# Optimization experiments

Hardware: AMD Instinct MI355X
Metric: run time of the kernel (lower is better)

Reference implementation:

```python
import jax, jax.numpy as jnp
import numpy as np

NUM_HEADS = 8
WEIGHTS_DIM = 512
INPUT_DIM = 512
D_HEAD = WEIGHTS_DIM // NUM_HEADS


def setup_inputs() -> dict:
    key = jax.random.key(0)
    ks = jax.random.split(key, 9)
    B, S, D = 4, 2048, INPUT_DIM
    s_in = 1.0 / np.sqrt(D)
    s_w = 1.0 / np.sqrt(WEIGHTS_DIM)
    return {
        "x": jax.random.normal(ks[0], (B, S, D), dtype=jnp.float32),
        "Wq": jax.random.normal(ks[1], (D, WEIGHTS_DIM), dtype=jnp.float32) * s_in,
        "bq": jnp.zeros((WEIGHTS_DIM,), dtype=jnp.float32),
        "Wk": jax.random.normal(ks[2], (D, WEIGHTS_DIM), dtype=jnp.float32) * s_in,
        "bk": jnp.zeros((WEIGHTS_DIM,), dtype=jnp.float32),
        "Wv": jax.random.normal(ks[3], (D, WEIGHTS_DIM), dtype=jnp.float32) * s_in,
        "bv": jnp.zeros((WEIGHTS_DIM,), dtype=jnp.float32),
        "Wh": jax.random.normal(ks[4], (WEIGHTS_DIM, D), dtype=jnp.float32) * s_w,
        "bh": jnp.zeros((D,), dtype=jnp.float32),
    }


def _split_heads(t):
    # [B, S, Dm] -> [B, H, S, d_head]
    B, S, _ = t.shape
    return t.reshape(B, S, NUM_HEADS, D_HEAD).transpose(0, 2, 1, 3)


def reference(x, Wq, bq, Wk, bk, Wv, bv, Wh, bh):
    q = _split_heads(x @ Wq + bq)
    k = _split_heads(x @ Wk + bk)
    v = _split_heads(x @ Wv + bv)
    scale = 1.0 / jnp.sqrt(jnp.float32(D_HEAD))
    scores = jnp.einsum("bhqd,bhkd->bhqk", q, k) * scale  # [B,H,S,S]
    weights = jax.nn.softmax(scores, axis=-1)
    attn = jnp.einsum("bhqk,bhkd->bhqd", weights, v)
    B, H, S, d = attn.shape
    concat = attn.transpose(0, 2, 1, 3).reshape(B, S, H * d)
    return concat @ Wh + bh
```

## Files before the change

kernel.cpp:

```cpp
#include <hip/hip_runtime.h>
#include <stdint.h>

#define NB  4
#define SS  2048
#define DD  512
#define HH  8
#define DHH 64
#define MM  (NB * SS)

typedef __attribute__((ext_vector_type(8))) short bf16x8;
typedef __attribute__((ext_vector_type(4))) float f32x4;
typedef __attribute__((ext_vector_type(4))) short s16x4;

union fu32 { float f; unsigned u; };
union pfu  { uint4 u; bf16x8 v; };

static __device__ __forceinline__ short f2bf(float f) {
  fu32 a; a.f = f;
  unsigned u = a.u;
  return (short)((u + 0x7fffu + ((u >> 16) & 1u)) >> 16);
}
static __device__ __forceinline__ float bf2f(short s) {
  fu32 t; t.u = ((unsigned)(unsigned short)s) << 16;
  return t.f;
}

static __device__ __forceinline__ void async16(const void* g, void* l) {
  __builtin_amdgcn_global_load_lds(
      (__attribute__((address_space(1))) unsigned*)(void*)g,
      (__attribute__((address_space(3))) unsigned*)l, 16, 0, 0);
}

__global__ __launch_bounds__(256) void prep_kernel(
    const float* __restrict__ x, short* __restrict__ xb,
    const float* __restrict__ W0, const float* __restrict__ W1,
    const float* __restrict__ W2, const float* __restrict__ W3,
    short* __restrict__ T0, short* __restrict__ T1,
    short* __restrict__ T2, short* __restrict__ T3) {
  const int bid = blockIdx.x, tid = threadIdx.x;
  if (bid < 2048) {
    int i = (bid * 256 + tid) * 8;
    float4 v0 = *(const float4*)(x + i);
    float4 v1 = *(const float4*)(x + i + 4);
    bf16x8 o;
    o[0] = f2bf(v0.x); o[1] = f2bf(v0.y); o[2] = f2bf(v0.z); o[3] = f2bf(v0.w);
    o[4] = f2bf(v1.x); o[5] = f2bf(v1.y); o[6] = f2bf(v1.z); o[7] = f2bf(v1.w);
    *(bf16x8*)(xb + i) = o;
  } else {
    int z = bid - 2048;
    int widx = z >> 6, rem = z & 63;
    const float* W = widx == 0 ? W0 : widx == 1 ? W1 : widx == 2 ? W2 : W3;
    short*       T = widx == 0 ? T0 : widx == 1 ? T1 : widx == 2 ? T2 : T3;
    int n  = (rem & 7) * 64 + (tid & 63);
    int k0 = (rem >> 3) * 64 + (tid >> 6) * 16;
    bf16x8 t0, t1;
#pragma unroll
    for (int j = 0; j < 8; ++j) t0[j] = f2bf(W[(size_t)(k0 + j) * DD + n]);
#pragma unroll
    for (int j = 0; j < 8; ++j) t1[j] = f2bf(W[(size_t)(k0 + 8 + j) * DD + n]);
    *(bf16x8*)(T + (size_t)n * DD + k0)     = t0;
    *(bf16x8*)(T + (size_t)n * DD + k0 + 8) = t1;
  }
}

__global__ __launch_bounds__(256, 4) void gemm_qkv_kernel(
    const short* __restrict__ A, const short* __restrict__ Bt,
    const float* __restrict__ bq, const float* __restrict__ bk,
    const float* __restrict__ bv, short* __restrict__ qout,
    short* __restrict__ kout, short* __restrict__ vtout, float qscale) {
  __shared__ __align__(16) short a_sh[64 * 64];
  __shared__ __align__(16) short b_sh[128 * 64];
  const int tid  = threadIdx.x;
  const int w    = tid >> 6, lane = tid & 63, quad = lane >> 4, l16 = lane & 15;
  const int m0   = blockIdx.y * 64, n0 = blockIdx.x * 128;
  const int mw   = (w >> 1) * 32,   nw = (w & 1) * 64;
  const int rw   = lane >> 3, seg = lane & 7, gs = seg ^ rw;
  const int sxz  = l16 & 7;

  f32x4 acc[2][4];
#pragma unroll
  for (int i = 0; i < 2; ++i)
#pragma unroll
    for (int j = 0; j < 4; ++j) acc[i][j] = {0.f, 0.f, 0.f, 0.f};

  for (int kt = 0; kt < DD; kt += 64) {
    __syncthreads();
    {
      const short* ga = A  + (size_t)(m0 + w * 16 + rw) * DD + kt + gs * 8;
      const short* gb = Bt + (size_t)(n0 + w * 32 + rw) * DD + kt + gs * 8;
#pragma unroll
      for (int i = 0; i < 2; ++i)
        async16(ga + (size_t)i * 8 * DD, &a_sh[(w * 16 + i * 8) * 64]);
#pragma unroll
      for (int i = 0; i < 4; ++i)
        async16(gb + (size_t)i * 8 * DD, &b_sh[(w * 32 + i * 8) * 64]);
    }
    __syncthreads();
#pragma unroll
    for (int ks = 0; ks < 2; ++ks) {
      const int so = ((ks * 4 + quad) ^ sxz) * 8;
      bf16x8 af[2], bfr[4];
#pragma unroll
      for (int mt = 0; mt < 2; ++mt)
        af[mt] = *(const bf16x8*)&a_sh[(mw + mt * 16 + l16) * 64 + so];
#pragma unroll
      for (int nt = 0; nt < 4; ++nt)
        bfr[nt] = *(const bf16x8*)&b_sh[(nw + nt * 16 + l16) * 64 + so];
#pragma unroll
      for (int mt = 0; mt < 2; ++mt)
#pragma unroll
        for (int nt = 0; nt < 4; ++nt)
          acc[mt][nt] = __builtin_amdgcn_mfma_f32_16x16x32_bf16(
              af[mt], bfr[nt], acc[mt][nt], 0, 0, 0);
    }
  }

#pragma unroll
  for (int nt = 0; nt < 4; ++nt) {
    const int n   = n0 + nw + nt * 16 + l16;
    const int sg  = n >> 9, n9 = n & 511, h = n9 >> 6, d = n & 63;
    const float bval = (sg == 0 ? bq : sg == 1 ? bk : bv)[n9];
    const float scl  = (sg == 0) ? qscale : 1.0f;
#pragma unroll
    for (int mt = 0; mt < 2; ++mt) {
      const int mb = m0 + mw + mt * 16 + quad * 4;
      const int bi = mb >> 11, s = mb & (SS - 1);
      if (sg == 2) {
        s16x4 pk;
#pragma unroll
        for (int r = 0; r < 4; ++r) pk[r] = f2bf(acc[mt][nt][r] + bval);
        *(s16x4*)&vtout[((size_t)(bi * HH + h) * DHH + d) * SS + s] = pk;
      } else {
        short* o = (sg == 0) ? qout : kout;
        const size_t base = ((size_t)(bi * HH + h) * SS + s) * DHH + d;
#pragma unroll
        for (int r = 0; r < 4; ++r)
          o[base + (size_t)r * DHH] = f2bf((acc[mt][nt][r] + bval) * scl);
      }
    }
  }
}

__global__ __launch_bounds__(256, 4) void attn_kernel(
    const short* __restrict__ Qa, const short* __restrict__ Ka,
    const short* __restrict__ Vt, short* __restrict__ Op0,
    short* __restrict__ Op1, float* __restrict__ lpw) {
  __shared__ __align__(16) short k_sh[128 * 64];
  __shared__ __align__(16) short vt_sh[64 * 128];

  const int tid  = threadIdx.x;
  const int w    = tid >> 6, lane = tid & 63, quad = lane >> 4, l16 = lane & 15;
  const int n    = blockIdx.x;
  const int grp  = (n & 7) * 8 + (n >> 7);
  const int qt_b = (n >> 3) & 15;
  const int half = grp & 1, h = (grp >> 1) & 7, b = grp >> 4;
  const int q0   = qt_b * 128;
  const int rw = lane >> 3, seg = lane & 7, gs = seg ^ rw;
  const int sxz = l16 & 7;
  const size_t base = (size_t)(b * HH + h) * SS * DHH;
  const short* Qg = Qa + base + (size_t)(q0 + w * 32) * DHH;
  const short* Kg = Ka + base;
  const short* Vg = Vt + base;

  bf16x8 qf[2][2];
#pragma unroll
  for (int mt = 0; mt < 2; ++mt)
#pragma unroll
    for (int ks = 0; ks < 2; ++ks)
      qf[mt][ks] = *(const bf16x8*)(Qg + (size_t)(mt * 16 + l16) * DHH + ks * 32 + quad * 8);

  bf16x8 ones;
#pragma unroll
  for (int j = 0; j < 8; ++j) ones[j] = (short)0x3F80;

  f32x4 o_acc[2][4];
#pragma unroll
  for (int qt = 0; qt < 2; ++qt)
#pragma unroll
    for (int dt = 0; dt < 4; ++dt) o_acc[qt][dt] = {0.f, 0.f, 0.f, 0.f};
  f32x4 l_acc[2] = {{0.f, 0.f, 0.f, 0.f}, {0.f, 0.f, 0.f, 0.f}};

  const int addrA = ((((quad & 1) << 1) + (quad >> 1)) * 16 + l16) * 4;
  const int addrB = addrA ^ 64;
  const bool qeven = (quad & 1) == 0;

  const int kstart = half * (SS / 2);

  for (int kb = kstart; kb < kstart + SS / 2; kb += 128) {
    __syncthreads();
    {
      const short* gk = Kg + (size_t)(kb + w * 32 + rw) * DHH + gs * 8;
#pragma unroll
      for (int i = 0; i < 4; ++i)
        async16(gk + (size_t)i * 8 * DHH, &k_sh[(w * 32 + i * 8) * 64]);
#pragma unroll
      for (int i = 0; i < 4; ++i) {
        const int d = w * 16 + i * 4 + (lane >> 4);
        const int gseg = (lane & 15) ^ (d & 15);
        async16(Vg + (size_t)d * SS + kb + gseg * 8,
                &vt_sh[(w * 16 + i * 4) * 128]);
      }
    }
    __syncthreads();

#pragma unroll
    for (int ck = 0; ck < 4; ++ck) {
      uint2 pk[2][2];
#pragma unroll
      for (int t = 0; t < 2; ++t) {
        const int knt = ck * 2 + t;
        bf16x8 kf0 = *(const bf16x8*)&k_sh[(knt * 16 + l16) * 64 + ((0 * 4 + quad) ^ sxz) * 8];
        bf16x8 kf1 = *(const bf16x8*)&k_sh[(knt * 16 + l16) * 64 + ((1 * 4 + quad) ^ sxz) * 8];
#pragma unroll
        for (int qt = 0; qt < 2; ++qt) {
          f32x4 s = {0.f, 0.f, 0.f, 0.f};
          s = __builtin_amdgcn_mfma_f32_16x16x32_bf16(kf0, qf[qt][0], s, 0, 0, 0);
          s = __builtin_amdgcn_mfma_f32_16x16x32_bf16(kf1, qf[qt][1], s, 0, 0, 0);
          fu32 e0, e1, e2, e3;
          e0.f = __builtin_amdgcn_exp2f(s[0]);
          e1.f = __builtin_amdgcn_exp2f(s[1]);
          e2.f = __builtin_amdgcn_exp2f(s[2]);
          e3.f = __builtin_amdgcn_exp2f(s[3]);
          pk[qt][t].x = __builtin_amdgcn_perm(e1.u, e0.u, 0x07060302u);
          pk[qt][t].y = __builtin_amdgcn_perm(e3.u, e2.u, 0x07060302u);
        }
      }
      pfu pf[2];
#pragma unroll
      for (int qt = 0; qt < 2; ++qt) {
        unsigned p1x = (unsigned)__shfl_xor((int)pk[qt][1].x, 16);
        unsigned p1y = (unsigned)__shfl_xor((int)pk[qt][1].y, 16);
        unsigned v0x = qeven ? pk[qt][0].x : p1x;
        unsigned v0y = qeven ? pk[qt][0].y : p1y;
        unsigned v2x = qeven ? p1x : pk[qt][0].x;
        unsigned v2y = qeven ? p1y : pk[qt][0].y;
        pf[qt].u.x = (unsigned)__builtin_amdgcn_ds_bpermute(addrA, (int)v0x);
        pf[qt].u.y = (unsigned)__builtin_amdgcn_ds_bpermute(addrA, (int)v0y);
        pf[qt].u.z = (unsigned)__builtin_amdgcn_ds_bpermute(addrB, (int)v2x);
        pf[qt].u.w = (unsigned)__builtin_amdgcn_ds_bpermute(addrB, (int)v2y);
        l_acc[qt] = __builtin_amdgcn_mfma_f32_16x16x32_bf16(pf[qt].v, ones, l_acc[qt], 0, 0, 0);
      }
#pragma unroll
      for (int dt = 0; dt < 4; ++dt) {
        bf16x8 vf = *(const bf16x8*)&vt_sh[(dt * 16 + l16) * 128 + ((ck * 4 + quad) ^ l16) * 8];
        o_acc[0][dt] = __builtin_amdgcn_mfma_f32_16x16x32_bf16(pf[0].v, vf, o_acc[0][dt], 0, 0, 0);
        o_acc[1][dt] = __builtin_amdgcn_mfma_f32_16x16x32_bf16(pf[1].v, vf, o_acc[1][dt], 0, 0, 0);
      }
    }
  }

  short* Op = half ? Op1 : Op0;
#pragma unroll
  for (int qt = 0; qt < 2; ++qt) {
#pragma unroll
    for (int r = 0; r < 4; ++r) {
      const int qg = q0 + w * 32 + qt * 16 + quad * 4 + r;
      const size_t row = (size_t)(b * HH + h) * SS + qg;
      if (l16 == 0)
        lpw[(size_t)half * (NB * HH * SS) + row] = l_acc[qt][r];
      const float inv = __builtin_amdgcn_rcpf(l_acc[qt][r]);
#pragma unroll
      for (int dt = 0; dt < 4; ++dt)
        Op[row * DHH + dt * 16 + l16] = f2bf(o_acc[qt][dt][r] * inv);
    }
  }
}

__global__ __launch_bounds__(256, 4) void gemm_proj_kernel(
    const short* __restrict__ Op0, const short* __restrict__ Op1,
    const float* __restrict__ lpw, const short* __restrict__ Bt,
    const float* __restrict__ bias, float* __restrict__ out) {
  __shared__ __align__(16) short a0_sh[64 * 64];
  __shared__ __align__(16) short a1_sh[64 * 64];
  __shared__ __align__(16) short b_sh[64 * 64];
  const int tid = threadIdx.x;
  const int w   = tid >> 6, lane = tid & 63, quad = lane >> 4, l16 = lane & 15;
  const int m0  = blockIdx.y * 64, n0 = blockIdx.x * 64;
  const int mw  = (w >> 1) * 32, nw = (w & 1) * 32;
  const int rw  = lane >> 3, seg = lane & 7, gs = seg ^ rw;
  const int sxz = l16 & 7;
  const int bb  = m0 >> 11, q0 = m0 & (SS - 1);

  f32x4 acc[2][2];
#pragma unroll
  for (int i = 0; i < 2; ++i)
#pragma unroll
    for (int j = 0; j < 2; ++j) acc[i][j] = {0.f, 0.f, 0.f, 0.f};

  for (int kt = 0; kt < DD; kt += 64) {
    const int h = kt >> 6;
    const size_t lbase = (size_t)(bb * HH + h) * SS + q0;
    const size_t abase = lbase * DHH;
    __syncthreads();
    {
      const short* g0 = Op0 + abase + (size_t)(w * 16 + rw) * DHH + gs * 8;
      const short* g1 = Op1 + abase + (size_t)(w * 16 + rw) * DHH + gs * 8;
      const short* gb = Bt + (size_t)(n0 + w * 16 + rw) * DD + kt + gs * 8;
#pragma unroll
      for (int i = 0; i < 2; ++i) {
        async16(g0 + (size_t)i * 8 * DHH, &a0_sh[(w * 16 + i * 8) * 64]);
        async16(g1 + (size_t)i * 8 * DHH, &a1_sh[(w * 16 + i * 8) * 64]);
        async16(gb + (size_t)i * 8 * DD,  &b_sh[(w * 16 + i * 8) * 64]);
      }
    }
    float w1[2], w2[2];
#pragma unroll
    for (int mt = 0; mt < 2; ++mt) {
      const size_t lrow = lbase + mw + mt * 16 + l16;
      const float l1 = lpw[lrow];
      const float l2 = lpw[(size_t)NB * HH * SS + lrow];
      const float inv = __builtin_amdgcn_rcpf(l1 + l2);
      w1[mt] = l1 * inv; w2[mt] = l2 * inv;
    }
    __syncthreads();
#pragma unroll
    for (int ks = 0; ks < 2; ++ks) {
      const int so = ((ks * 4 + quad) ^ sxz) * 8;
      pfu af[2];
#pragma unroll
      for (int mt = 0; mt < 2; ++mt) {
        bf16x8 a0 = *(const bf16x8*)&a0_sh[(mw + mt * 16 + l16) * 64 + so];
        bf16x8 a1 = *(const bf16x8*)&a1_sh[(mw + mt * 16 + l16) * 64 + so];
        unsigned* rp = (unsigned*)&af[mt];
#pragma unroll
        for (int jp = 0; jp < 4; ++jp) {
          fu32 f0, f1;
          f0.f = w1[mt] * bf2f(a0[2 * jp])     + w2[mt] * bf2f(a1[2 * jp]);
          f1.f = w1[mt] * bf2f(a0[2 * jp + 1]) + w2[mt] * bf2f(a1[2 * jp + 1]);
          rp[jp] = __builtin_amdgcn_perm(f1.u, f0.u, 0x07060302u);
        }
      }
#pragma unroll
      for (int nt = 0; nt < 2; ++nt) {
        bf16x8 bfr = *(const bf16x8*)&b_sh[(nw + nt * 16 + l16) * 64 + so];
        acc[0][nt] = __builtin_amdgcn_mfma_f32_16x16x32_bf16(af[0].v, bfr, acc[0][nt], 0, 0, 0);
        acc[1][nt] = __builtin_amdgcn_mfma_f32_16x16x32_bf16(af[1].v, bfr, acc[1][nt], 0, 0, 0);
      }
    }
  }

#pragma unroll
  for (int nt = 0; nt < 2; ++nt) {
    const int   n  = n0 + nw + nt * 16 + l16;
    const float bv = bias[n];
#pragma unroll
    for (int mt = 0; mt < 2; ++mt)
#pragma unroll
      for (int r = 0; r < 4; ++r) {
        const int m = m0 + mw + mt * 16 + quad * 4 + r;
        out[(size_t)m * DD + n] = acc[mt][nt][r] + bv;
      }
  }
}

extern "C" void kernel_launch(void* const* d_in, const int* in_sizes, int n_in,
                              void* d_out, int out_size, void* d_ws, size_t ws_size,
                              hipStream_t stream) {
  (void)in_sizes; (void)n_in; (void)out_size; (void)ws_size;
  const float* x  = (const float*)d_in[0];
  const float* Wq = (const float*)d_in[1];
  const float* bq = (const float*)d_in[2];
  const float* Wk = (const float*)d_in[3];
  const float* bk = (const float*)d_in[4];
  const float* Wv = (const float*)d_in[5];
  const float* bv = (const float*)d_in[6];
  const float* Wh = (const float*)d_in[7];
  const float* bh = (const float*)d_in[8];

  short* ws  = (short*)d_ws;
  short* xb  = ws;
  short* wqt = xb  + (size_t)MM * DD;
  short* wkt = wqt + (size_t)DD * DD;
  short* wvt = wkt + (size_t)DD * DD;
  short* wht = wvt + (size_t)DD * DD;
  short* qws = wht + (size_t)DD * DD;
  short* kws = qws + (size_t)MM * DD;
  short* vws = kws + (size_t)MM * DD;
  short* op1 = vws + (size_t)MM * DD;
  float* lpw = (float*)(op1 + (size_t)MM * DD);

  hipLaunchKernelGGL(prep_kernel, dim3(2048 + 256), dim3(256), 0, stream,
                     x, xb, Wq, Wk, Wv, Wh, wqt, wkt, wvt, wht);

  const float qscale = 1.4426950408889634f / 8.0f;
  hipLaunchKernelGGL(gemm_qkv_kernel, dim3(12, 128), dim3(256), 0, stream,
                     xb, wqt, bq, bk, bv, qws, kws, vws, qscale);

  hipLaunchKernelGGL(attn_kernel, dim3(1024), dim3(256), 0, stream,
                     qws, kws, vws, xb, op1, lpw);

  hipLaunchKernelGGL(gemm_proj_kernel, dim3(8, 128), dim3(256), 0, stream,
                     xb, op1, lpw, wht, bh, (float*)d_out);
}
```

Before: 172.8 us.

## Double query rows per attention block to halve K/V tile reloads

Each attention block now covers 256 query rows (64 per wave) instead of 128, so every K and V tile staged in shared memory feeds twice as many MFMAs. The grid shrinks from 1024 to 512 blocks and the launch bound drops to 2 waves per SIMD to allow the larger accumulator and Q-fragment register footprint. V fragments are hoisted and reused across the four query tiles. The cost is higher register pressure, lower occupancy and fewer blocks for the 256 CUs to share.

```diff
diff --git a/kernel.cpp b/kernel.cpp
--- a/kernel.cpp
+++ b/kernel.cpp
@@ -141,7 +141,7 @@
   }
 }
 
-__global__ __launch_bounds__(256, 4) void attn_kernel(
+__global__ __launch_bounds__(256, 2) void attn_kernel(
     const short* __restrict__ Qa, const short* __restrict__ Ka,
     const short* __restrict__ Vt, short* __restrict__ Op0,
     short* __restrict__ Op1, float* __restrict__ lpw) {
@@ -151,34 +151,36 @@
   const int tid  = threadIdx.x;
   const int w    = tid >> 6, lane = tid & 63, quad = lane >> 4, l16 = lane & 15;
   const int n    = blockIdx.x;
-  const int grp  = (n & 7) * 8 + (n >> 7);
-  const int qt_b = (n >> 3) & 15;
+  const int grp  = (n & 7) * 8 + ((n >> 3) & 7);
+  const int qt_b = n >> 6;
   const int half = grp & 1, h = (grp >> 1) & 7, b = grp >> 4;
-  const int q0   = qt_b * 128;
+  const int q0   = qt_b * 256;
   const int rw = lane >> 3, seg = lane & 7, gs = seg ^ rw;
   const int sxz = l16 & 7;
   const size_t base = (size_t)(b * HH + h) * SS * DHH;
-  const short* Qg = Qa + base + (size_t)(q0 + w * 32) * DHH;
+  const short* Qg = Qa + base + (size_t)(q0 + w * 64) * DHH;
   const short* Kg = Ka + base;
   const short* Vg = Vt + base;
 
-  bf16x8 qf[2][2];
-#pragma unroll
-  for (int mt = 0; mt < 2; ++mt)
+  bf16x8 qf[4][2];
+#pragma unroll
+  for (int qt = 0; qt < 4; ++qt)
 #pragma unroll
     for (int ks = 0; ks < 2; ++ks)
-      qf[mt][ks] = *(const bf16x8*)(Qg + (size_t)(mt * 16 + l16) * DHH + ks * 32 + quad * 8);
+      qf[qt][ks] = *(const bf16x8*)(Qg + (size_t)(qt * 16 + l16) * DHH + ks * 32 + quad * 8);
 
   bf16x8 ones;
 #pragma unroll
   for (int j = 0; j < 8; ++j) ones[j] = (short)0x3F80;
 
-  f32x4 o_acc[2][4];
-#pragma unroll
-  for (int qt = 0; qt < 2; ++qt)
+  f32x4 o_acc[4][4];
+#pragma unroll
+  for (int qt = 0; qt < 4; ++qt)
 #pragma unroll
     for (int dt = 0; dt < 4; ++dt) o_acc[qt][dt] = {0.f, 0.f, 0.f, 0.f};
-  f32x4 l_acc[2] = {{0.f, 0.f, 0.f, 0.f}, {0.f, 0.f, 0.f, 0.f}};
+  f32x4 l_acc[4];
+#pragma unroll
+  for (int qt = 0; qt < 4; ++qt) l_acc[qt] = {0.f, 0.f, 0.f, 0.f};
 
   const int addrA = ((((quad & 1) << 1) + (quad >> 1)) * 16 + l16) * 4;
   const int addrB = addrA ^ 64;
@@ -205,14 +207,14 @@
 
 #pragma unroll
     for (int ck = 0; ck < 4; ++ck) {
-      uint2 pk[2][2];
+      uint2 pk[4][2];
 #pragma unroll
       for (int t = 0; t < 2; ++t) {
         const int knt = ck * 2 + t;
         bf16x8 kf0 = *(const bf16x8*)&k_sh[(knt * 16 + l16) * 64 + ((0 * 4 + quad) ^ sxz) * 8];
         bf16x8 kf1 = *(const bf16x8*)&k_sh[(knt * 16 + l16) * 64 + ((1 * 4 + quad) ^ sxz) * 8];
 #pragma unroll
-        for (int qt = 0; qt < 2; ++qt) {
+        for (int qt = 0; qt < 4; ++qt) {
           f32x4 s = {0.f, 0.f, 0.f, 0.f};
           s = __builtin_amdgcn_mfma_f32_16x16x32_bf16(kf0, qf[qt][0], s, 0, 0, 0);
           s = __builtin_amdgcn_mfma_f32_16x16x32_bf16(kf1, qf[qt][1], s, 0, 0, 0);
@@ -225,36 +227,37 @@
           pk[qt][t].y = __builtin_amdgcn_perm(e3.u, e2.u, 0x07060302u);
         }
       }
-      pfu pf[2];
-#pragma unroll
-      for (int qt = 0; qt < 2; ++qt) {
+      bf16x8 vf[4];
+#pragma unroll
+      for (int dt = 0; dt < 4; ++dt)
+        vf[dt] = *(const bf16x8*)&vt_sh[(dt * 16 + l16) * 128 + ((ck * 4 + quad) ^ l16) * 8];
+#pragma unroll
+      for (int qt = 0; qt < 4; ++qt) {
         unsigned p1x = (unsigned)__shfl_xor((int)pk[qt][1].x, 16);
         unsigned p1y = (unsigned)__shfl_xor((int)pk[qt][1].y, 16);
         unsigned v0x = qeven ? pk[qt][0].x : p1x;
         unsigned v0y = qeven ? pk[qt][0].y : p1y;
         unsigned v2x = qeven ? p1x : pk[qt][0].x;
         unsigned v2y = qeven ? p1y : pk[qt][0].y;
-        pf[qt].u.x = (unsigned)__builtin_amdgcn_ds_bpermute(addrA, (int)v0x);
-        pf[qt].u.y = (unsigned)__builtin_amdgcn_ds_bpermute(addrA, (int)v0y);
-        pf[qt].u.z = (unsigned)__builtin_amdgcn_ds_bpermute(addrB, (int)v2x);
-        pf[qt].u.w = (unsigned)__builtin_amdgcn_ds_bpermute(addrB, (int)v2y);
-        l_acc[qt] = __builtin_amdgcn_mfma_f32_16x16x32_bf16(pf[qt].v, ones, l_acc[qt], 0, 0, 0);
-      }
-#pragma unroll
-      for (int dt = 0; dt < 4; ++dt) {
-        bf16x8 vf = *(const bf16x8*)&vt_sh[(dt * 16 + l16) * 128 + ((ck * 4 + quad) ^ l16) * 8];
-        o_acc[0][dt] = __builtin_amdgcn_mfma_f32_16x16x32_bf16(pf[0].v, vf, o_acc[0][dt], 0, 0, 0);
-        o_acc[1][dt] = __builtin_amdgcn_mfma_f32_16x16x32_bf16(pf[1].v, vf, o_acc[1][dt], 0, 0, 0);
+        pfu pf;
+        pf.u.x = (unsigned)__builtin_amdgcn_ds_bpermute(addrA, (int)v0x);
+        pf.u.y = (unsigned)__builtin_amdgcn_ds_bpermute(addrA, (int)v0y);
+        pf.u.z = (unsigned)__builtin_amdgcn_ds_bpermute(addrB, (int)v2x);
+        pf.u.w = (unsigned)__builtin_amdgcn_ds_bpermute(addrB, (int)v2y);
+        l_acc[qt] = __builtin_amdgcn_mfma_f32_16x16x32_bf16(pf.v, ones, l_acc[qt], 0, 0, 0);
+#pragma unroll
+        for (int dt = 0; dt < 4; ++dt)
+          o_acc[qt][dt] = __builtin_amdgcn_mfma_f32_16x16x32_bf16(pf.v, vf[dt], o_acc[qt][dt], 0, 0, 0);
       }
     }
   }
 
   short* Op = half ? Op1 : Op0;
 #pragma unroll
-  for (int qt = 0; qt < 2; ++qt) {
+  for (int qt = 0; qt < 4; ++qt) {
 #pragma unroll
     for (int r = 0; r < 4; ++r) {
-      const int qg = q0 + w * 32 + qt * 16 + quad * 4 + r;
+      const int qg = q0 + w * 64 + qt * 16 + quad * 4 + r;
       const size_t row = (size_t)(b * HH + h) * SS + qg;
       if (l16 == 0)
         lpw[(size_t)half * (NB * HH * SS) + row] = l_acc[qt][r];
@@ -386,7 +389,7 @@
   hipLaunchKernelGGL(gemm_qkv_kernel, dim3(12, 128), dim3(256), 0, stream,
                      xb, wqt, bq, bk, bv, qws, kws, vws, qscale);
 
-  hipLaunchKernelGGL(attn_kernel, dim3(1024), dim3(256), 0, stream,
+  hipLaunchKernelGGL(attn_kernel, dim3(512), dim3(256), 0, stream,
                      qws, kws, vws, xb, op1, lpw);
 
   hipLaunchKernelGGL(gemm_proj_kernel, dim3(8, 128), dim3(256), 0, stream,
```

After: 177.1 us. +2.5%, slower.
